# Optimization experiments

Measured on AMD Instinct MI355X. Metric: run time of the kernel, lower is better.

The kernel has to match this reference:

```python
import jax, jax.numpy as jnp
import numpy as np

# static config (must match init_kwargs)
B, HIS, N, DIN = 16, 13, 400, 16
HID, S, PRED, LAYERS = 256, 4, 12, 3
NG = S * N  # nodes in the combined virtual graph
DEG = 8     # avg out-degree of base adjacency
EPS = 1e-5


def _build_graph():
    """Reproduce _combine_graph (offset bug included) + edge weights."""
    rng = np.random.default_rng(0)
    cols = np.argsort(rng.random((N, N)), axis=1)[:, :DEG]  # [N, DEG] distinct cols per row
    w = rng.uniform(0.1, 1.0, size=(N, DEG)).astype(np.float32)
    rows = np.repeat(np.arange(N), DEG)
    c = cols.ravel()
    off = (S - 1) * N
    # first block rows: [adj | adj]; last diagonal block: adj
    src = np.concatenate([rows, rows, rows + off]).astype(np.int32)
    dst = np.concatenate([c, c + N, c + off]).astype(np.int32)
    ew = np.concatenate([w.ravel(), w.ravel(), w.ravel()]).astype(np.float32)
    return src, dst, ew


def _checkpoints():
    mark, chp = S, []
    while mark < HIS:
        chp.append(mark)
        mark += S - 1
    if chp[-1] != HIS:
        chp.append(HIS)
    return chp


def setup_inputs() -> dict:
    key = jax.random.key(0)
    ks = jax.random.split(key, 9)
    src, dst, ew = _build_graph()
    sc = 0.05
    return {
        "inputs": jax.random.normal(ks[0], (B, HIS, N, DIN), jnp.float32),
        "W_in": jax.random.normal(ks[1], (DIN, HID), jnp.float32) * sc,
        "b_in": jax.random.normal(ks[2], (HID,), jnp.float32) * sc,
        "gcn_W": jax.random.normal(ks[3], (LAYERS, HID, HID), jnp.float32) * sc,
        "gcn_b": jax.random.normal(ks[4], (LAYERS, HID), jnp.float32) * sc,
        "W1": jax.random.normal(ks[5], (1, PRED), jnp.float32) * sc,
        "b1": jax.random.normal(ks[6], (PRED,), jnp.float32) * sc,
        "W2": jax.random.normal(ks[7], (HID, 1), jnp.float32) * sc,
        "b2": jax.random.normal(ks[8], (1,), jnp.float32) * sc,
        "edge_w": jnp.asarray(ew),
        "src": jnp.asarray(src),
        "dst": jnp.asarray(dst),
    }


def _gcn(h, src, dst, edge_w, inv_out, inv_in, gcn_W, gcn_b):
    """LAYERS-deep GraphConv (norm='both', edge weights), ReLU between layers.
    h: [B, NG, HID]. Dropout is identity (eval)."""
    seg = jax.vmap(lambda m: jax.ops.segment_sum(m, dst, num_segments=NG))
    for i in range(LAYERS):
        hs = h * inv_out[None, :, None]          # D_out^{-1/2} on src side
        msg = hs[:, src, :] * edge_w[None, :, None]  # [B, E, HID]
        agg = seg(msg) * inv_in[None, :, None]   # D_in^{-1/2} on dst side
        h_new = agg @ gcn_W[i] + gcn_b[i]
        h = jax.nn.relu(h_new) if i < LAYERS - 1 else h_new
    return h


def reference(inputs, W_in, b_in, gcn_W, gcn_b, W1, b1, W2, b2, edge_w, src, dst):
    # unweighted degrees for symmetric normalization (guard isolated nodes)
    ones = jnp.ones_like(edge_w)
    out_deg = jnp.zeros((NG,), jnp.float32).at[src].add(ones)
    in_deg = jnp.zeros((NG,), jnp.float32).at[dst].add(ones)
    inv_out = jax.lax.rsqrt(jnp.maximum(out_deg, 1.0))
    inv_in = jax.lax.rsqrt(jnp.maximum(in_deg, 1.0))

    x = inputs @ W_in + b_in  # [B, HIS, N, HID]
    last = None
    left = 0
    for idx, right in enumerate(_checkpoints()):
        if idx == 0:
            fs = x[:, left:right]                       # [B, S, N, HID]
        else:
            fs = jnp.concatenate([last, x[:, left:right]], axis=1)
        h = fs.reshape(B, NG, HID)
        res = h
        h = _gcn(h, src, dst, edge_w, inv_out, inv_in, gcn_W, gcn_b) + res
        # nn.LayerNorm([B*S*N, HID], elementwise_affine=False) on a tensor of
        # exactly that shape => normalize over ALL elements jointly
        h = (h - h.mean()) * jax.lax.rsqrt(h.var() + EPS)
        h = h.reshape(B, S, N, HID)
        last = h[:, -1:, :, :]  # [B, 1, N, HID]
        left = right

    t = jnp.transpose(last, (0, 3, 2, 1))   # [B, HID, N, 1]
    o = t @ W1 + b1                          # [B, HID, N, PRED]
    o = jnp.transpose(o, (0, 3, 2, 1))       # [B, PRED, N, HID]
    o = jax.nn.relu(o)
    return o @ W2 + b2                       # [B, PRED, N, 1]
```

## Files before the change

### kernel.cpp

```cpp
#include <hip/hip_runtime.h>

#define BB 16
#define HIS 13
#define NN 400
#define DIN 16
#define HID 256
#define PRED 12
#define NE 9600
#define EPSF 1e-5f
#define HSZ ((size_t)25600*256)
#define BAND ((size_t)NN*BB*HID)
#define ROWS_BAND (NN*BB)
#define CSR_CAP 4608

typedef __attribute__((ext_vector_type(8))) short short8v;
typedef __attribute__((ext_vector_type(4))) float f32x4;

__device__ __forceinline__ short f2bf(float x) {
    unsigned u = __float_as_uint(x);
    return (short)((u + 0x7FFF + ((u >> 16) & 1)) >> 16);
}
__device__ __forceinline__ float bf2f(short x) {
    return __uint_as_float(((unsigned)(unsigned short)x) << 16);
}
__device__ __forceinline__ void gload16(const void* g, void* l) {
    __builtin_amdgcn_global_load_lds((const __attribute__((address_space(1))) void*)g,
                                     (__attribute__((address_space(3))) void*)l,
                                     16, 0, 0);
}

__global__ __launch_bounds__(256) void k_graph(
    const int* __restrict__ src, const int* __restrict__ dst,
    const float* __restrict__ ew, const float* __restrict__ gcn_W,
    float* __restrict__ inv_in, float* __restrict__ csum,
    int* __restrict__ csr_off, int* __restrict__ csr_src,
    float* __restrict__ cf1, float* __restrict__ cf2,
    short* __restrict__ Wt, float* __restrict__ stats)
{
    __shared__ int odeg[1600];
    __shared__ int ideg[400];
    __shared__ int cnt[400];
    __shared__ int offl[401];
    __shared__ int scan_t[256];
    __shared__ float csuml[400];
    __shared__ float S[64][65];
    int t = threadIdx.x, bi = blockIdx.x;
    if (bi == 0) {
        for (int g = t; g < 1600; g += 256) odeg[g] = 0;
        for (int g = t; g < 400; g += 256) { ideg[g] = 0; cnt[g] = 0; csuml[g] = 0.f; }
        if (t < 9) stats[t] = 0.f;
        if (t == 9) stats[9] = (1.0f - EPSF) * (float)HSZ;
        __syncthreads();
        for (int e = t; e < NE; e += 256) atomicAdd(&odeg[src[e]], 1);
        for (int e = t; e < 3200; e += 256) atomicAdd(&ideg[dst[e]], 1);
        __syncthreads();
        int s = 0, p0 = 0, p1 = 0;
        if (t < 200) {
            p0 = (ideg[2 * t] + 3) & ~3;
            p1 = (ideg[2 * t + 1] + 3) & ~3;
            s = p0 + p1;
        }
        scan_t[t] = s;
        __syncthreads();
        for (int o = 1; o < 256; o <<= 1) {
            int v = (t >= o) ? scan_t[t - o] : 0;
            __syncthreads();
            scan_t[t] += v;
            __syncthreads();
        }
        if (t < 200) { int base = scan_t[t] - s; offl[2 * t] = base; offl[2 * t + 1] = base + p0; }
        if (t == 255) offl[400] = scan_t[255];
        __syncthreads();
        int cap = offl[400];
        for (int g = t; g < 401; g += 256) csr_off[g] = offl[g];
        for (int g = t; g < 400; g += 256) inv_in[g] = rsqrtf(fmaxf((float)ideg[g], 1.f));
        for (int i = t; i < cap; i += 256) { csr_src[i] = 0; cf1[i] = 0.f; cf2[i] = 0.f; }
        __syncthreads();
        for (int e = t; e < 3200; e += 256) {
            int d = dst[e];
            int r = src[e];
            int p = offl[d] + atomicAdd(&cnt[d], 1);
            float w = ew[e];
            float c1 = w * rsqrtf(fmaxf((float)odeg[r], 1.f));
            float c2 = w * rsqrtf(fmaxf((float)odeg[1200 + r], 1.f));
            csr_src[p] = r;
            cf1[p] = c1;
            cf2[p] = c2;
            atomicAdd(&csuml[d], c1);
        }
        __syncthreads();
        for (int g = t; g < 400; g += 256) csum[g] = csuml[g];
    } else {
        int tile = bi - 1;
        int l = tile / 16, sub = tile % 16;
        int k0 = (sub >> 2) * 64, n0 = (sub & 3) * 64;
        int tr = t >> 6, tc = t & 63;
#pragma unroll
        for (int i = 0; i < 16; ++i) {
            int r = i * 4 + tr;
            S[r][tc] = gcn_W[(size_t)l * 65536 + (size_t)(k0 + r) * 256 + n0 + tc];
        }
        __syncthreads();
#pragma unroll
        for (int i = 0; i < 16; ++i) {
            int n = i * 4 + tr;
            Wt[(size_t)l * 65536 + (size_t)(n0 + n) * 256 + k0 + tc] = f2bf(S[tc][n]);
        }
    }
}

__global__ __launch_bounds__(256) void k_xproj(
    const float* __restrict__ inp, const float* __restrict__ W_in,
    const float* __restrict__ b_in, const float* __restrict__ gb2,
    short* __restrict__ xproj, float* __restrict__ stats)
{
    __shared__ float Wl[16 * 256];
    __shared__ float xs[256];
    __shared__ short stg[16 * 256];
    __shared__ float red[512];
    int t = threadIdx.x, bi = blockIdx.x;
    int time = bi / 400, n = bi % 400;
#pragma unroll
    for (int i = 0; i < 16; ++i) Wl[i * 256 + t] = W_in[i * 256 + t];
    { int b = t >> 4, d = t & 15;
      xs[t] = inp[(((size_t)b * HIS + time) * NN + n) * DIN + d]; }
    __syncthreads();
    float acc[16];
    float bv = b_in[t];
#pragma unroll
    for (int b = 0; b < 16; ++b) acc[b] = bv;
#pragma unroll
    for (int d = 0; d < 16; ++d) {
        float w = Wl[d * 256 + t];
#pragma unroll
        for (int b = 0; b < 16; ++b) acc[b] = fmaf(xs[b * 16 + d], w, acc[b]);
    }
    bool isStat = (time == 2 || time == 5 || time == 8 || time == 11);
    if (isStat) {
        float gb = gb2[t];
        float s1 = 0.f, s2 = 0.f;
#pragma unroll
        for (int b = 0; b < 16; ++b) {
            float v = acc[b] + gb;
            s1 += v; s2 += v * v;
        }
        red[t] = s1; red[256 + t] = s2;
        __syncthreads();
        for (int o = 128; o > 0; o >>= 1) {
            if (t < o) { red[t] += red[t + o]; red[256 + t] += red[256 + t + o]; }
            __syncthreads();
        }
        if (t == 0) {
            int it = (time - 2) / 3;
            atomicAdd(&stats[it * 2], red[0]);
            atomicAdd(&stats[it * 2 + 1], red[256]);
        }
    } else {
#pragma unroll
        for (int b = 0; b < 16; ++b) stg[b * 256 + t] = f2bf(acc[b]);
        __syncthreads();
        int b = t >> 4, c = (t & 15) * 16;
        size_t gbase = (size_t)time * BAND + ((size_t)n * 16 + b) * HID + c;
        *(short8v*)&xproj[gbase]     = *(short8v*)&stg[b * 256 + c];
        *(short8v*)&xproj[gbase + 8] = *(short8v*)&stg[b * 256 + c + 8];
    }
}

template <int MODE>
__global__ __launch_bounds__(256) void k_layer(
    const short* __restrict__ hX, const short* __restrict__ hY,
    const float* __restrict__ stA, const float* __restrict__ csum,
    const float* __restrict__ inv_in, const int* __restrict__ csr_off,
    const int* __restrict__ csr_src, const float* __restrict__ cf1,
    const float* __restrict__ cf2,
    const short* __restrict__ Bt, const float* __restrict__ bias,
    const short* __restrict__ resX0, const float* __restrict__ stR,
    const short* __restrict__ resX1, const short* __restrict__ resY,
    short* __restrict__ C, float* __restrict__ stats)
{
    __shared__ short As[64][264];
    __shared__ short Bs[2][8192];
    __shared__ float red[512];
    int tid = threadIdx.x;
    int wid = tid >> 6, l = tid & 63;
    int l15 = l & 15, l4 = l >> 4;
    int blk = blockIdx.x;
    int isY = blk >= 100;
    int gl = (isY ? blk - 100 : blk) * 4;
    int rowL0 = gl * 16;
    int wn = wid * 64;
    const short* hsrc = isY ? hY : hX;
    const float* cf = isY ? cf2 : cf1;

    float am = 1.f, moff = 0.f;
    if (MODE == 0 && !isY) {
        float mean = stA[0] * (1.f / (float)HSZ);
        float var  = stA[1] * (1.f / (float)HSZ) - mean * mean;
        float istd = rsqrtf(var + EPSF);
        am = istd; moff = mean * istd;
    }

    int br = l >> 2;
    int kd = (l & 3) ^ ((br >> 1) & 3);
    for (int ch = wid; ch < 16; ch += 4)
        gload16(Bt + ((size_t)(ch * 16 + br)) * 256 + kd * 8, &Bs[0][ch * 512]);

    {
        int b = tid >> 4, hsc = (tid & 15) * 16;
        const size_t lane_off = (size_t)b * HID + hsc;
        for (int gi = 0; gi < 4; ++gi) {
            int g = gl + gi;
            int beg = csr_off[g], end = csr_off[g + 1];
            float acc[16];
#pragma unroll
            for (int i = 0; i < 16; ++i) acc[i] = 0.f;
            for (int j = beg; j < end; j += 4) {
                int ss[4]; float cc[4];
#pragma unroll
                for (int u = 0; u < 4; ++u) { ss[u] = csr_src[j + u]; cc[u] = cf[j + u]; }
                short8v va[4], vb[4];
#pragma unroll
                for (int u = 0; u < 4; ++u) {
                    const short8v* q = (const short8v*)&hsrc[(size_t)ss[u] * 4096 + lane_off];
                    va[u] = q[0]; vb[u] = q[1];
                }
#pragma unroll
                for (int u = 0; u < 4; ++u) {
#pragma unroll
                    for (int i = 0; i < 8; ++i) {
                        acc[i]     = fmaf(cc[u], bf2f(va[u][i]), acc[i]);
                        acc[8 + i] = fmaf(cc[u], bf2f(vb[u][i]), acc[8 + i]);
                    }
                }
            }
            float s = inv_in[g];
            float addv = (MODE == 0 && !isY) ? (-moff * csum[g]) : 0.f;
            short8v o0, o1;
#pragma unroll
            for (int i = 0; i < 8; ++i) o0[i] = f2bf(s * fmaf(am, acc[i], addv));
#pragma unroll
            for (int i = 0; i < 8; ++i) o1[i] = f2bf(s * fmaf(am, acc[8 + i], addv));
            int row = gi * 16 + b;
            *(short8v*)&As[row][hsc]     = o0;
            *(short8v*)&As[row][hsc + 8] = o1;
        }
    }
    __syncthreads();

    f32x4 cacc[4][4] = {};
    int xsw = (l4 ^ ((l15 >> 1) & 3)) * 8;
    for (int kc = 0; kc < 8; ++kc) {
        int cur = kc & 1;
        if (kc < 7) {
            int k0n = (kc + 1) * 32;
            for (int ch = wid; ch < 16; ch += 4)
                gload16(Bt + ((size_t)(ch * 16 + br)) * 256 + k0n + kd * 8,
                        &Bs[cur ^ 1][ch * 512]);
        }
        int k0 = kc * 32;
        short8v av[4], bv[4];
#pragma unroll
        for (int mi = 0; mi < 4; ++mi)
            av[mi] = *(const short8v*)&As[mi * 16 + l15][k0 + l4 * 8];
#pragma unroll
        for (int ni = 0; ni < 4; ++ni)
            bv[ni] = *(const short8v*)&Bs[cur][(wn + ni * 16 + l15) * 32 + xsw];
#pragma unroll
        for (int mi = 0; mi < 4; ++mi)
#pragma unroll
            for (int ni = 0; ni < 4; ++ni)
                cacc[mi][ni] = __builtin_amdgcn_mfma_f32_16x16x32_bf16(
                    av[mi], bv[ni], cacc[mi][ni], 0, 0, 0);
        __syncthreads();
    }

    if (MODE <= 1) {
#pragma unroll
        for (int ni = 0; ni < 4; ++ni) {
            int col = wn + ni * 16 + l15;
            float bvv = bias[col];
#pragma unroll
            for (int mi = 0; mi < 4; ++mi) {
#pragma unroll
                for (int r = 0; r < 4; ++r) {
                    float v = fmaxf(cacc[mi][ni][r] + bvv, 0.f);
                    As[mi * 16 + l4 * 4 + r][col] = f2bf(v);
                }
            }
        }
        __syncthreads();
        int row = tid >> 2, cs = (tid & 3) * 64;
        size_t gb = ((size_t)(isY ? ROWS_BAND : 0) + rowL0 + row) * HID + cs;
#pragma unroll
        for (int i = 0; i < 8; ++i)
            *(short8v*)&C[gb + i * 8] = *(const short8v*)&As[row][cs + i * 8];
    } else {
        float s1 = 0.f, s2 = 0.f;
        if (!isY) {
            float meanR = stR[0] * (1.f / (float)HSZ);
            float varR  = stR[1] * (1.f / (float)HSZ) - meanR * meanR;
            float istdR = rsqrtf(varR + EPSF);
#pragma unroll
            for (int ni = 0; ni < 4; ++ni) {
                int col = wn + ni * 16 + l15;
                float bvv = bias[col];
#pragma unroll
                for (int mi = 0; mi < 4; ++mi) {
#pragma unroll
                    for (int r = 0; r < 4; ++r) {
                        int rowg = rowL0 + mi * 16 + l4 * 4 + r;
                        size_t ix = (size_t)rowg * HID + col;
                        float base = cacc[mi][ni][r] + bvv;
                        float v1 = base + (bf2f(resX0[ix]) - meanR) * istdR;
                        float v2 = base + bf2f(resX1[ix]);
                        s1 += v1 + v2;
                        s2 += v1 * v1 + v2 * v2;
                    }
                }
            }
        } else {
#pragma unroll
            for (int ni = 0; ni < 4; ++ni) {
                int col = wn + ni * 16 + l15;
                float bvv = bias[col];
#pragma unroll
                for (int mi = 0; mi < 4; ++mi) {
#pragma unroll
                    for (int r = 0; r < 4; ++r) {
                        int rowl = mi * 16 + l4 * 4 + r;
                        size_t ix = (size_t)(rowL0 + rowl) * HID + col;
                        float v = cacc[mi][ni][r] + bvv + bf2f(resY[ix]);
                        s1 += v; s2 += v * v;
                        As[rowl][col] = f2bf(v);
                    }
                }
            }
            __syncthreads();
            int row = tid >> 2, cs = (tid & 3) * 64;
            size_t gb = (size_t)(rowL0 + row) * HID + cs;
#pragma unroll
            for (int i = 0; i < 8; ++i)
                *(short8v*)&C[gb + i * 8] = *(const short8v*)&As[row][cs + i * 8];
        }
        red[tid] = s1; red[256 + tid] = s2;
        __syncthreads();
        for (int o = 128; o > 0; o >>= 1) {
            if (tid < o) { red[tid] += red[tid + o]; red[256 + tid] += red[256 + tid + o]; }
            __syncthreads();
        }
        if (tid == 0) { atomicAdd(&stats[0], red[0]); atomicAdd(&stats[1], red[256]); }
    }
}

__global__ void k_head(const short* __restrict__ hlast, const float* __restrict__ st,
                       const float* __restrict__ W1, const float* __restrict__ b1,
                       const float* __restrict__ W2, const float* __restrict__ b2,
                       float* __restrict__ out) {
    float mean = st[0] * (1.0f / (float)HSZ);
    float var  = st[1] * (1.0f / (float)HSZ) - mean * mean;
    float istd = rsqrtf(var + EPSF);
    int n = blockIdx.x, b = blockIdx.y, tid = threadIdx.x;
    float v  = (bf2f(hlast[((size_t)n * BB + b) * HID + tid]) - mean) * istd;
    float w2 = W2[tid];
    float b2v = b2[0];
    __shared__ float ps[4];
    for (int p = 0; p < PRED; ++p) {
        float t = fmaxf(fmaf(v, W1[p], b1[p]), 0.f) * w2;
#pragma unroll
        for (int o = 32; o > 0; o >>= 1) t += __shfl_down(t, o, 64);
        int wid = tid >> 6, lane = tid & 63;
        if (lane == 0) ps[wid] = t;
        __syncthreads();
        if (tid == 0) out[(size_t)(b * PRED + p) * NN + n] = ps[0] + ps[1] + ps[2] + ps[3] + b2v;
        __syncthreads();
    }
}

extern "C" void kernel_launch(void* const* d_in, const int* in_sizes, int n_in,
                              void* d_out, int out_size, void* d_ws, size_t ws_size,
                              hipStream_t stream) {
    const float* inp   = (const float*)d_in[0];
    const float* W_in  = (const float*)d_in[1];
    const float* b_in  = (const float*)d_in[2];
    const float* gcn_W = (const float*)d_in[3];
    const float* gcn_b = (const float*)d_in[4];
    const float* W1    = (const float*)d_in[5];
    const float* b1    = (const float*)d_in[6];
    const float* W2    = (const float*)d_in[7];
    const float* b2    = (const float*)d_in[8];
    const float* ew    = (const float*)d_in[9];
    const int*   src   = (const int*)d_in[10];
    const int*   dst   = (const int*)d_in[11];
    float* out = (float*)d_out;

    char* w = (char*)d_ws;
    auto alloc = [&](size_t bytes) {
        char* p = w;
        w += (bytes + 255) & ~(size_t)255;
        return p;
    };
    short* hA    = (short*)alloc((size_t)2 * ROWS_BAND * HID * 2);
    short* hB    = (short*)alloc((size_t)2 * ROWS_BAND * HID * 2);
    short* hl0   = (short*)alloc(BAND * 2);
    short* hl1   = (short*)alloc(BAND * 2);
    short* xproj = (short*)alloc((size_t)13 * BAND * 2);
    short* Wt    = (short*)alloc((size_t)3 * 65536 * 2);
    float* inv_in  = (float*)alloc(400 * 4);
    float* csum    = (float*)alloc(400 * 4);
    int*   csr_off = (int*)alloc(401 * 4);
    int*   csr_srcv= (int*)alloc(CSR_CAP * 4);
    float* cf1     = (float*)alloc(CSR_CAP * 4);
    float* cf2     = (float*)alloc(CSR_CAP * 4);
    float* stats   = (float*)alloc(12 * 4);

    k_graph<<<49, 256, 0, stream>>>(src, dst, ew, gcn_W, inv_in, csum, csr_off,
                                    csr_srcv, cf1, cf2, Wt, stats);
    k_xproj<<<5200, 256, 0, stream>>>(inp, W_in, b_in, gcn_b + 512, xproj, stats);

    short* hlbuf[2] = {hl0, hl1};
    const int lefts[4] = {0, 4, 7, 10};
    const size_t RB = (size_t)ROWS_BAND * HID;
    for (int it = 0; it < 4; ++it) {
        int t1 = (it == 0) ? 1 : lefts[it];
        int t3 = (it == 0) ? 3 : lefts[it] + 2;
        const short* hlp = (it == 0) ? xproj : hlbuf[(it - 1) & 1];
        const float* stA = (it == 0) ? stats + 8 : stats + (it - 1) * 2;
        short* cur = hlbuf[it & 1];
        k_layer<0><<<200, 256, 0, stream>>>(hlp, xproj + (size_t)t3 * BAND, stA, csum,
                                            inv_in, csr_off, csr_srcv, cf1, cf2,
                                            Wt, gcn_b,
                                            nullptr, nullptr, nullptr, nullptr,
                                            hA, nullptr);
        k_layer<1><<<200, 256, 0, stream>>>(hA, hA + RB, stats + 8, csum,
                                            inv_in, csr_off, csr_srcv, cf1, cf2,
                                            Wt + 65536, gcn_b + 256,
                                            nullptr, nullptr, nullptr, nullptr,
                                            hB, nullptr);
        k_layer<2><<<200, 256, 0, stream>>>(hB, hB + RB, stats + 8, csum,
                                            inv_in, csr_off, csr_srcv, cf1, cf2,
                                            Wt + 131072, gcn_b + 512,
                                            hlp, stA, xproj + (size_t)t1 * BAND,
                                            xproj + (size_t)t3 * BAND,
                                            cur, stats + it * 2);
    }

    k_head<<<dim3(NN, BB), 256, 0, stream>>>(hlbuf[1], stats + 6, W1, b1, W2, b2, out);
}
```

Measured before the change: 327.5 us.

## Fuse graph prep with input projection and halve layer tile rows

Merges the graph/weight-preparation kernel and the input projection into one launch, and moves the stats zeroing to a memset. The projection now has each block handle four nodes with W_in held in registers and wave-shuffle reductions. The GCN layer kernel now processes 32 rows per block instead of 64, doubling the grid to 400 blocks to occupy more CUs. The CSR padding rises to multiples of 8 so the gather loop can unroll 8 neighbours per iteration. The trade-offs are less MFMA work per block, more redundant B-tile loads, and uncoalesced per-thread scalar input reads in the projection.

```diff
diff --git a/kernel.cpp b/kernel.cpp
--- a/kernel.cpp
+++ b/kernel.cpp
@@ -11,7 +11,7 @@
 #define HSZ ((size_t)25600*256)
 #define BAND ((size_t)NN*BB*HID)
 #define ROWS_BAND (NN*BB)
-#define CSR_CAP 4608
+#define CSR_CAP 6144
 
 typedef __attribute__((ext_vector_type(8))) short short8v;
 typedef __attribute__((ext_vector_type(4))) float f32x4;
@@ -29,26 +29,28 @@
                                      16, 0, 0);
 }
 
-__global__ __launch_bounds__(256) void k_graph(
+__global__ __launch_bounds__(256) void k_prep(
     const int* __restrict__ src, const int* __restrict__ dst,
     const float* __restrict__ ew, const float* __restrict__ gcn_W,
+    const float* __restrict__ inp, const float* __restrict__ W_in,
+    const float* __restrict__ b_in, const float* __restrict__ gb2,
     float* __restrict__ inv_in, float* __restrict__ csum,
     int* __restrict__ csr_off, int* __restrict__ csr_src,
     float* __restrict__ cf1, float* __restrict__ cf2,
-    short* __restrict__ Wt, float* __restrict__ stats)
+    short* __restrict__ Wt, short* __restrict__ xproj,
+    float* __restrict__ stats)
 {
-    __shared__ int odeg[1600];
-    __shared__ int ideg[400];
-    __shared__ int cnt[400];
-    __shared__ int offl[401];
-    __shared__ int scan_t[256];
-    __shared__ float csuml[400];
-    __shared__ float S[64][65];
+    __shared__ __align__(16) char SM[17408];
     int t = threadIdx.x, bi = blockIdx.x;
     if (bi == 0) {
+        int* odeg = (int*)SM;
+        int* ideg = odeg + 1600;
+        int* cnt  = ideg + 400;
+        int* offl = cnt + 400;
+        int* scan_t = offl + 401;
+        float* csuml = (float*)(scan_t + 256);
         for (int g = t; g < 1600; g += 256) odeg[g] = 0;
         for (int g = t; g < 400; g += 256) { ideg[g] = 0; cnt[g] = 0; csuml[g] = 0.f; }
-        if (t < 9) stats[t] = 0.f;
         if (t == 9) stats[9] = (1.0f - EPSF) * (float)HSZ;
         __syncthreads();
         for (int e = t; e < NE; e += 256) atomicAdd(&odeg[src[e]], 1);
@@ -56,8 +58,8 @@
         __syncthreads();
         int s = 0, p0 = 0, p1 = 0;
         if (t < 200) {
-            p0 = (ideg[2 * t] + 3) & ~3;
-            p1 = (ideg[2 * t + 1] + 3) & ~3;
+            p0 = (ideg[2 * t] + 7) & ~7;
+            p1 = (ideg[2 * t + 1] + 7) & ~7;
             s = p0 + p1;
         }
         scan_t[t] = s;
@@ -90,7 +92,8 @@
         }
         __syncthreads();
         for (int g = t; g < 400; g += 256) csum[g] = csuml[g];
-    } else {
+    } else if (bi <= 48) {
+        float (*S)[65] = (float(*)[65])SM;
         int tile = bi - 1;
         int l = tile / 16, sub = tile % 16;
         int k0 = (sub >> 2) * 64, n0 = (sub & 3) * 64;
@@ -106,63 +109,56 @@
             int n = i * 4 + tr;
             Wt[(size_t)l * 65536 + (size_t)(n0 + n) * 256 + k0 + tc] = f2bf(S[tc][n]);
         }
-    }
-}
-
-__global__ __launch_bounds__(256) void k_xproj(
-    const float* __restrict__ inp, const float* __restrict__ W_in,
-    const float* __restrict__ b_in, const float* __restrict__ gb2,
-    short* __restrict__ xproj, float* __restrict__ stats)
-{
-    __shared__ float Wl[16 * 256];
-    __shared__ float xs[256];
-    __shared__ short stg[16 * 256];
-    __shared__ float red[512];
-    int t = threadIdx.x, bi = blockIdx.x;
-    int time = bi / 400, n = bi % 400;
-#pragma unroll
-    for (int i = 0; i < 16; ++i) Wl[i * 256 + t] = W_in[i * 256 + t];
-    { int b = t >> 4, d = t & 15;
-      xs[t] = inp[(((size_t)b * HIS + time) * NN + n) * DIN + d]; }
-    __syncthreads();
-    float acc[16];
-    float bv = b_in[t];
-#pragma unroll
-    for (int b = 0; b < 16; ++b) acc[b] = bv;
-#pragma unroll
-    for (int d = 0; d < 16; ++d) {
-        float w = Wl[d * 256 + t];
-#pragma unroll
-        for (int b = 0; b < 16; ++b) acc[b] = fmaf(xs[b * 16 + d], w, acc[b]);
-    }
-    bool isStat = (time == 2 || time == 5 || time == 8 || time == 11);
-    if (isStat) {
-        float gb = gb2[t];
+    } else {
+        float* rbuf = (float*)SM;
+        float wr[16];
+#pragma unroll
+        for (int d = 0; d < 16; ++d) wr[d] = W_in[d * 256 + t];
+        float bvv = b_in[t];
+        int job0 = (bi - 49) * 4;
+        int time = job0 / 400;
+        int n0 = job0 % 400;
+        bool isStat = (time == 2 || time == 5 || time == 8 || time == 11);
+        float gb = isStat ? gb2[t] : 0.f;
         float s1 = 0.f, s2 = 0.f;
-#pragma unroll
-        for (int b = 0; b < 16; ++b) {
-            float v = acc[b] + gb;
-            s1 += v; s2 += v * v;
-        }
-        red[t] = s1; red[256 + t] = s2;
-        __syncthreads();
-        for (int o = 128; o > 0; o >>= 1) {
-            if (t < o) { red[t] += red[t + o]; red[256 + t] += red[256 + t + o]; }
+        for (int j = 0; j < 4; ++j) {
+            int n = n0 + j;
+            float acc[16];
+#pragma unroll
+            for (int b = 0; b < 16; ++b) acc[b] = bvv;
+#pragma unroll
+            for (int b = 0; b < 16; ++b) {
+                const float* xr = inp + (((size_t)b * HIS + time) * NN + n) * DIN;
+#pragma unroll
+                for (int d = 0; d < 16; ++d) acc[b] = fmaf(xr[d], wr[d], acc[b]);
+            }
+            if (isStat) {
+#pragma unroll
+                for (int b = 0; b < 16; ++b) {
+                    float v = acc[b] + gb;
+                    s1 += v; s2 += v * v;
+                }
+            } else {
+                size_t gbase = (size_t)time * BAND + ((size_t)n * 16) * 256 + t;
+#pragma unroll
+                for (int b = 0; b < 16; ++b) xproj[gbase + (size_t)b * 256] = f2bf(acc[b]);
+            }
+        }
+        if (isStat) {
+#pragma unroll
+            for (int o = 32; o > 0; o >>= 1) {
+                s1 += __shfl_down(s1, o, 64);
+                s2 += __shfl_down(s2, o, 64);
+            }
+            int wid = t >> 6, lane = t & 63;
+            if (lane == 0) { rbuf[wid] = s1; rbuf[4 + wid] = s2; }
             __syncthreads();
-        }
-        if (t == 0) {
-            int it = (time - 2) / 3;
-            atomicAdd(&stats[it * 2], red[0]);
-            atomicAdd(&stats[it * 2 + 1], red[256]);
-        }
-    } else {
-#pragma unroll
-        for (int b = 0; b < 16; ++b) stg[b * 256 + t] = f2bf(acc[b]);
-        __syncthreads();
-        int b = t >> 4, c = (t & 15) * 16;
-        size_t gbase = (size_t)time * BAND + ((size_t)n * 16 + b) * HID + c;
-        *(short8v*)&xproj[gbase]     = *(short8v*)&stg[b * 256 + c];
-        *(short8v*)&xproj[gbase + 8] = *(short8v*)&stg[b * 256 + c + 8];
+            if (t == 0) {
+                int it = (time - 2) / 3;
+                atomicAdd(&stats[it * 2],     rbuf[0] + rbuf[1] + rbuf[2] + rbuf[3]);
+                atomicAdd(&stats[it * 2 + 1], rbuf[4] + rbuf[5] + rbuf[6] + rbuf[7]);
+            }
+        }
     }
 }
 
@@ -178,15 +174,15 @@
     const short* __restrict__ resX1, const short* __restrict__ resY,
     short* __restrict__ C, float* __restrict__ stats)
 {
-    __shared__ short As[64][264];
+    __shared__ short As[32][264];
     __shared__ short Bs[2][8192];
     __shared__ float red[512];
     int tid = threadIdx.x;
     int wid = tid >> 6, l = tid & 63;
     int l15 = l & 15, l4 = l >> 4;
     int blk = blockIdx.x;
-    int isY = blk >= 100;
-    int gl = (isY ? blk - 100 : blk) * 4;
+    int isY = blk >= 200;
+    int gl = (isY ? blk - 200 : blk) * 2;
     int rowL0 = gl * 16;
     int wn = wid * 64;
     const short* hsrc = isY ? hY : hX;
@@ -208,24 +204,24 @@
     {
         int b = tid >> 4, hsc = (tid & 15) * 16;
         const size_t lane_off = (size_t)b * HID + hsc;
-        for (int gi = 0; gi < 4; ++gi) {
+        for (int gi = 0; gi < 2; ++gi) {
             int g = gl + gi;
             int beg = csr_off[g], end = csr_off[g + 1];
             float acc[16];
 #pragma unroll
             for (int i = 0; i < 16; ++i) acc[i] = 0.f;
-            for (int j = beg; j < end; j += 4) {
-                int ss[4]; float cc[4];
-#pragma unroll
-                for (int u = 0; u < 4; ++u) { ss[u] = csr_src[j + u]; cc[u] = cf[j + u]; }
-                short8v va[4], vb[4];
-#pragma unroll
-                for (int u = 0; u < 4; ++u) {
+            for (int j = beg; j < end; j += 8) {
+                int ss[8]; float cc[8];
+#pragma unroll
+                for (int u = 0; u < 8; ++u) { ss[u] = csr_src[j + u]; cc[u] = cf[j + u]; }
+                short8v va[8], vb[8];
+#pragma unroll
+                for (int u = 0; u < 8; ++u) {
                     const short8v* q = (const short8v*)&hsrc[(size_t)ss[u] * 4096 + lane_off];
                     va[u] = q[0]; vb[u] = q[1];
                 }
 #pragma unroll
-                for (int u = 0; u < 4; ++u) {
+                for (int u = 0; u < 8; ++u) {
 #pragma unroll
                     for (int i = 0; i < 8; ++i) {
                         acc[i]     = fmaf(cc[u], bf2f(va[u][i]), acc[i]);
@@ -247,7 +243,7 @@
     }
     __syncthreads();
 
-    f32x4 cacc[4][4] = {};
+    f32x4 cacc[2][4] = {};
     int xsw = (l4 ^ ((l15 >> 1) & 3)) * 8;
     for (int kc = 0; kc < 8; ++kc) {
         int cur = kc & 1;
@@ -258,15 +254,15 @@
                         &Bs[cur ^ 1][ch * 512]);
         }
         int k0 = kc * 32;
-        short8v av[4], bv[4];
-#pragma unroll
-        for (int mi = 0; mi < 4; ++mi)
+        short8v av[2], bv[4];
+#pragma unroll
+        for (int mi = 0; mi < 2; ++mi)
             av[mi] = *(const short8v*)&As[mi * 16 + l15][k0 + l4 * 8];
 #pragma unroll
         for (int ni = 0; ni < 4; ++ni)
             bv[ni] = *(const short8v*)&Bs[cur][(wn + ni * 16 + l15) * 32 + xsw];
 #pragma unroll
-        for (int mi = 0; mi < 4; ++mi)
+        for (int mi = 0; mi < 2; ++mi)
 #pragma unroll
             for (int ni = 0; ni < 4; ++ni)
                 cacc[mi][ni] = __builtin_amdgcn_mfma_f32_16x16x32_bf16(
@@ -280,7 +276,7 @@
             int col = wn + ni * 16 + l15;
             float bvv = bias[col];
 #pragma unroll
-            for (int mi = 0; mi < 4; ++mi) {
+            for (int mi = 0; mi < 2; ++mi) {
 #pragma unroll
                 for (int r = 0; r < 4; ++r) {
                     float v = fmaxf(cacc[mi][ni][r] + bvv, 0.f);
@@ -289,10 +285,10 @@
             }
         }
         __syncthreads();
-        int row = tid >> 2, cs = (tid & 3) * 64;
+        int row = tid >> 3, cs = (tid & 7) * 32;
         size_t gb = ((size_t)(isY ? ROWS_BAND : 0) + rowL0 + row) * HID + cs;
 #pragma unroll
-        for (int i = 0; i < 8; ++i)
+        for (int i = 0; i < 4; ++i)
             *(short8v*)&C[gb + i * 8] = *(const short8v*)&As[row][cs + i * 8];
     } else {
         float s1 = 0.f, s2 = 0.f;
@@ -305,7 +301,7 @@
                 int col = wn + ni * 16 + l15;
                 float bvv = bias[col];
 #pragma unroll
-                for (int mi = 0; mi < 4; ++mi) {
+                for (int mi = 0; mi < 2; ++mi) {
 #pragma unroll
                     for (int r = 0; r < 4; ++r) {
                         int rowg = rowL0 + mi * 16 + l4 * 4 + r;
@@ -324,7 +320,7 @@
                 int col = wn + ni * 16 + l15;
                 float bvv = bias[col];
 #pragma unroll
-                for (int mi = 0; mi < 4; ++mi) {
+                for (int mi = 0; mi < 2; ++mi) {
 #pragma unroll
                     for (int r = 0; r < 4; ++r) {
                         int rowl = mi * 16 + l4 * 4 + r;
@@ -336,10 +332,10 @@
                 }
             }
             __syncthreads();
-            int row = tid >> 2, cs = (tid & 3) * 64;
+            int row = tid >> 3, cs = (tid & 7) * 32;
             size_t gb = (size_t)(rowL0 + row) * HID + cs;
 #pragma unroll
-            for (int i = 0; i < 8; ++i)
+            for (int i = 0; i < 4; ++i)
                 *(short8v*)&C[gb + i * 8] = *(const short8v*)&As[row][cs + i * 8];
         }
         red[tid] = s1; red[256 + tid] = s2;
@@ -413,9 +409,10 @@
     float* cf2     = (float*)alloc(CSR_CAP * 4);
     float* stats   = (float*)alloc(12 * 4);
 
-    k_graph<<<49, 256, 0, stream>>>(src, dst, ew, gcn_W, inv_in, csum, csr_off,
-                                    csr_srcv, cf1, cf2, Wt, stats);
-    k_xproj<<<5200, 256, 0, stream>>>(inp, W_in, b_in, gcn_b + 512, xproj, stats);
+    hipMemsetAsync(stats, 0, 12 * 4, stream);
+    k_prep<<<1349, 256, 0, stream>>>(src, dst, ew, gcn_W, inp, W_in, b_in,
+                                     gcn_b + 512, inv_in, csum, csr_off,
+                                     csr_srcv, cf1, cf2, Wt, xproj, stats);
 
     short* hlbuf[2] = {hl0, hl1};
     const int lefts[4] = {0, 4, 7, 10};
@@ -426,17 +423,17 @@
         const short* hlp = (it == 0) ? xproj : hlbuf[(it - 1) & 1];
         const float* stA = (it == 0) ? stats + 8 : stats + (it - 1) * 2;
         short* cur = hlbuf[it & 1];
-        k_layer<0><<<200, 256, 0, stream>>>(hlp, xproj + (size_t)t3 * BAND, stA, csum,
+        k_layer<0><<<400, 256, 0, stream>>>(hlp, xproj + (size_t)t3 * BAND, stA, csum,
                                             inv_in, csr_off, csr_srcv, cf1, cf2,
                                             Wt, gcn_b,
                                             nullptr, nullptr, nullptr, nullptr,
                                             hA, nullptr);
-        k_layer<1><<<200, 256, 0, stream>>>(hA, hA + RB, stats + 8, csum,
+        k_layer<1><<<400, 256, 0, stream>>>(hA, hA + RB, stats + 8, csum,
                                             inv_in, csr_off, csr_srcv, cf1, cf2,
                                             Wt + 65536, gcn_b + 256,
                                             nullptr, nullptr, nullptr, nullptr,
                                             hB, nullptr);
-        k_layer<2><<<200, 256, 0, stream>>>(hB, hB + RB, stats + 8, csum,
+        k_layer<2><<<400, 256, 0, stream>>>(hB, hB + RB, stats + 8, csum,
                                             inv_in, csr_off, csr_srcv, cf1, cf2,
                                             Wt + 131072, gcn_b + 512,
                                             hlp, stA, xproj + (size_t)t1 * BAND,
```

After: 287.9 us. 12.1% less time.
